# Performance work log

Hardware: AMD Instinct MI355X
Metric: run time of the kernel (lower is better)

The kernel has to match this reference:

```python
import jax, jax.numpy as jnp
import numpy as np

# FlowNetC correlation config: kernel_size=1, so no kernel-window averaging;
# pad_size == max_displacement -> output spatial size == input spatial size.
B, C, H, W = 8, 256, 48, 64
MAX_DISP = 20   # max_displacement
STRIDE2 = 2     # displacement stride
PAD = 20        # pad_size
GRID_RAD = MAX_DISP // STRIDE2            # 10
GRID_W = 2 * GRID_RAD + 1                 # 21 -> 441 displacement channels


def setup_inputs() -> dict:
    key = jax.random.key(0)
    k1, k2 = jax.random.split(key)
    return {
        "input1": jax.random.normal(k1, (B, C, H, W), dtype=jnp.float32),
        "input2": jax.random.normal(k2, (B, C, H, W), dtype=jnp.float32),
    }


def _correlation(input1, input2):
    b, c, h, w = input1.shape
    p2 = jnp.pad(input2, ((0, 0), (0, 0), (PAD, PAD), (PAD, PAD)))
    # Displacement start offsets into the padded map. dy-major ordering matches
    # the CUDA kernel: top_channel = dy_idx * GRID_W + dx_idx.
    d = np.arange(-GRID_RAD, GRID_RAD + 1) * STRIDE2 + PAD  # [21]
    offs = np.stack(np.meshgrid(d, d, indexing="ij"), axis=-1).reshape(-1, 2)
    offs = jnp.asarray(offs, dtype=jnp.int32)  # [441, 2] (dy, dx)
    sumelems = jnp.float32(c)  # kernel_size^2 * C with kernel_size=1

    def step(carry, o):
        shifted = jax.lax.dynamic_slice(p2, (0, 0, o[0], o[1]), (b, c, h, w))
        # mean over channels of elementwise product -> [B, H, W]
        return carry, jnp.sum(input1 * shifted, axis=1) / sumelems

    _, ys = jax.lax.scan(step, 0, offs)          # [441, B, H, W]
    return jnp.transpose(ys, (1, 0, 2, 3))       # [B, 441, H, W]


def reference(input1, input2):
    return _correlation(input1, input2)
```

## Files before the change

### kernel.cpp

```cpp
#include <hip/hip_runtime.h>

typedef __bf16 bf16x8 __attribute__((ext_vector_type(8)));
typedef float f32x4 __attribute__((ext_vector_type(4)));
typedef float f32x16 __attribute__((ext_vector_type(16)));

#define CC 256
#define HH 48
#define WW 64
#define HW (HH * WW)
#define NB 8
#define GW 21

__global__ __launch_bounds__(256) void prep_kernel(const float* __restrict__ in1,
                                                   const float* __restrict__ in2,
                                                   unsigned short* __restrict__ o1,
                                                   unsigned short* __restrict__ o2)
{
    __shared__ float lds[CC * 33];
    int blk  = blockIdx.x;
    int sel  = (blk >= 768);
    int blk2 = sel ? blk - 768 : blk;
    int b  = blk2 & 7;
    int st = blk2 >> 3;
    int s0 = st * 32;
    const float* src = sel ? in2 : in1;
    unsigned short* dst = sel ? o2 : o1;
    float scale = sel ? 1.0f : (1.0f / 256.0f);

    int t = threadIdx.x;
    int sidx  = t & 31;
    int cbase = t >> 5;
    const float* sb = src + (size_t)b * CC * HW + s0;
    #pragma unroll
    for (int p = 0; p < 32; ++p) {
        int c = cbase + p * 8;
        lds[c * 33 + sidx] = sb[(size_t)c * HW + sidx] * scale;
    }
    __syncthreads();

    int y  = s0 >> 6;
    int xb = s0 & 63;
    int s  = t & 31;
    int c8 = t >> 5;
    unsigned short* db = dst + (size_t)(b * HH + y) * 32 * 64 * 8;
    #pragma unroll
    for (int it = 0; it < 4; ++it) {
        int cblk = it * 8 + c8;
        unsigned dw[4];
        #pragma unroll
        for (int d = 0; d < 4; ++d) {
            unsigned u0 = __builtin_bit_cast(unsigned, lds[(cblk * 8 + 2 * d) * 33 + s]);
            u0 += 0x7fffu + ((u0 >> 16) & 1u);
            unsigned u1 = __builtin_bit_cast(unsigned, lds[(cblk * 8 + 2 * d + 1) * 33 + s]);
            u1 += 0x7fffu + ((u1 >> 16) & 1u);
            dw[d] = (u0 >> 16) | (u1 & 0xffff0000u);
        }
        *(uint4*)(db + ((size_t)cblk * 64 + xb + s) * 8) =
            make_uint4(dw[0], dw[1], dw[2], dw[3]);
    }
}

__global__ __launch_bounds__(256, 4) void corr_kernel(const unsigned short* __restrict__ in1F,
                                                      const unsigned short* __restrict__ in2F,
                                                      float* __restrict__ out)
{
    __shared__ float dbuf[4 * 2304];
    int blk  = blockIdx.x;
    int b    = blk & 7;
    int t2   = blk >> 3;
    int ysrc = (t2 % 88) - 20;
    int jg   = t2 / 88;
    int tid  = threadIdx.x;
    int w    = tid >> 6;
    int lane = tid & 63;

    int j = jg * 4 + w;
    if (j > 20) return;
    int yo = ysrc - 2 * (j - 10);
    if (yo < 0 || yo >= HH) return;

    float* orow = out + (((size_t)(b * 441 + j * GW)) * HH + yo) * WW;

    if (ysrc < 0 || ysrc >= HH) {
        #pragma unroll
        for (int jx = 0; jx < GW; ++jx)
            orow[(size_t)jx * HW + lane] = 0.0f;
        return;
    }

    int l31 = lane & 31;
    int q2  = lane >> 5;

    const unsigned short* arow =
        in1F + (((size_t)(b * HH + yo) * 32 + q2) * 64 + l31) * 8;
    const unsigned short* brow =
        in2F + (((size_t)(b * HH + ysrc) * 32 + q2) * 64 + l31) * 8;

    f32x16 acc[2][2];
    #pragma unroll
    for (int mt = 0; mt < 2; ++mt)
        #pragma unroll
        for (int nt = 0; nt < 2; ++nt)
            acc[mt][nt] = (f32x16)(0.0f);

    bf16x8 Af[2][2], Bf[2][2];
    #pragma unroll
    for (int mt = 0; mt < 2; ++mt)
        Af[0][mt] = *(const bf16x8*)(arow + mt * 32 * 8);
    #pragma unroll
    for (int nt = 0; nt < 2; ++nt)
        Bf[0][nt] = *(const bf16x8*)(brow + nt * 32 * 8);

    #pragma unroll
    for (int kk = 0; kk < 16; ++kk) {
        int cur = kk & 1, nxt = cur ^ 1;
        if (kk < 15) {
            #pragma unroll
            for (int mt = 0; mt < 2; ++mt)
                Af[nxt][mt] = *(const bf16x8*)(arow + (size_t)(kk + 1) * 1024 + mt * 32 * 8);
            #pragma unroll
            for (int nt = 0; nt < 2; ++nt)
                Bf[nxt][nt] = *(const bf16x8*)(brow + (size_t)(kk + 1) * 1024 + nt * 32 * 8);
        }
        #pragma unroll
        for (int mt = 0; mt < 2; ++mt)
            #pragma unroll
            for (int nt = 0; nt < 2; ++nt)
                acc[mt][nt] = __builtin_amdgcn_mfma_f32_32x32x16_bf16(
                    Af[cur][mt], Bf[cur][nt], acc[mt][nt], 0, 0, 0);
    }

    float* dtw = dbuf + w * 2304;
    #pragma unroll
    for (int h = 0; h < 2; ++h) {
        #pragma unroll
        for (int nt = 0; nt < 2; ++nt) {
            #pragma unroll
            for (int rq = 0; rq < 4; ++rq) {
                f32x4 v = { acc[h][nt][4 * rq], acc[h][nt][4 * rq + 1],
                            acc[h][nt][4 * rq + 2], acc[h][nt][4 * rq + 3] };
                *(f32x4*)(dtw + (nt * 32 + l31) * 36 + rq * 8 + q2 * 4) = v;
            }
        }
        int x = h * 32 + l31;
        #pragma unroll
        for (int jj = 0; jj < 11; ++jj) {
            int jx = 2 * jj + q2;
            if (jx >= GW) continue;
            int colx = x + 2 * (jx - 10);
            float v = (colx >= 0 && colx < WW) ? dtw[colx * 36 + l31] : 0.0f;
            orow[(size_t)jx * HW + x] = v;
        }
    }
}

extern "C" void kernel_launch(void* const* d_in, const int* in_sizes, int n_in,
                              void* d_out, int out_size, void* d_ws, size_t ws_size,
                              hipStream_t stream)
{
    (void)in_sizes; (void)n_in; (void)out_size; (void)ws_size;
    const float* in1 = (const float*)d_in[0];
    const float* in2 = (const float*)d_in[1];
    float* out = (float*)d_out;

    unsigned short* in1F = (unsigned short*)d_ws;
    unsigned short* in2F = in1F + (size_t)NB * HW * CC;

    prep_kernel<<<dim3(1536), dim3(256), 0, stream>>>(in1, in2, in1F, in2F);
    corr_kernel<<<dim3(NB * 88 * 6), dim3(256), 0, stream>>>(in1F, in2F, out);
}
```

Baseline: 118.4 us.

## Stage shared input2 row in LDS, deepen A prefetch, use nontemporal stores

All four waves in a block share the same input2 row, so that 32KB row is now loaded cooperatively into LDS once per block and the B fragments are read from LDS instead of global memory. The A operand prefetch is deepened to three buffers to hide more global latency. Output stores become nontemporal to avoid polluting the cache. The change adds two block-wide barriers, keeps invalid waves alive until those barriers, and reuses the same LDS for the transpose staging.

```diff
diff --git a/kernel.cpp b/kernel.cpp
--- a/kernel.cpp
+++ b/kernel.cpp
@@ -64,7 +64,9 @@
                                                       const unsigned short* __restrict__ in2F,
                                                       float* __restrict__ out)
 {
-    __shared__ float dbuf[4 * 2304];
+    __shared__ unsigned char smem[36864];
+    unsigned short* Bl = (unsigned short*)smem;
+
     int blk  = blockIdx.x;
     int b    = blk & 7;
     int t2   = blk >> 3;
@@ -74,63 +76,86 @@
     int w    = tid >> 6;
     int lane = tid & 63;
 
-    int j = jg * 4 + w;
-    if (j > 20) return;
+    int j  = jg * 4 + w;
     int yo = ysrc - 2 * (j - 10);
-    if (yo < 0 || yo >= HH) return;
+    bool jvalid = (j <= 20) && (yo >= 0) && (yo < HH);
 
-    float* orow = out + (((size_t)(b * 441 + j * GW)) * HH + yo) * WW;
+    float* orow = jvalid
+        ? out + (((size_t)(b * 441 + j * GW)) * HH + yo) * WW
+        : out;
 
     if (ysrc < 0 || ysrc >= HH) {
-        #pragma unroll
-        for (int jx = 0; jx < GW; ++jx)
-            orow[(size_t)jx * HW + lane] = 0.0f;
+        if (jvalid) {
+            #pragma unroll
+            for (int jx = 0; jx < GW; ++jx)
+                __builtin_nontemporal_store(0.0f, orow + (size_t)jx * HW + lane);
+        }
         return;
     }
+
+    {
+        const unsigned short* bsrc = in2F + (size_t)(b * HH + ysrc) * (32 * 64 * 8);
+        #pragma unroll
+        for (int it = 0; it < 8; ++it) {
+            size_t off = ((size_t)it * 256 + tid) * 8;
+            *(uint4*)(Bl + off) = *(const uint4*)(bsrc + off);
+        }
+    }
+    __syncthreads();
 
     int l31 = lane & 31;
     int q2  = lane >> 5;
 
-    const unsigned short* arow =
-        in1F + (((size_t)(b * HH + yo) * 32 + q2) * 64 + l31) * 8;
-    const unsigned short* brow =
-        in2F + (((size_t)(b * HH + ysrc) * 32 + q2) * 64 + l31) * 8;
+    f32x16 acc[2][2];
+    if (jvalid) {
+        const unsigned short* arow =
+            in1F + (((size_t)(b * HH + yo) * 32 + q2) * 64 + l31) * 8;
+        const unsigned short* brow = Bl + ((size_t)q2 * 64 + l31) * 8;
 
-    f32x16 acc[2][2];
-    #pragma unroll
-    for (int mt = 0; mt < 2; ++mt)
-        #pragma unroll
-        for (int nt = 0; nt < 2; ++nt)
-            acc[mt][nt] = (f32x16)(0.0f);
-
-    bf16x8 Af[2][2], Bf[2][2];
-    #pragma unroll
-    for (int mt = 0; mt < 2; ++mt)
-        Af[0][mt] = *(const bf16x8*)(arow + mt * 32 * 8);
-    #pragma unroll
-    for (int nt = 0; nt < 2; ++nt)
-        Bf[0][nt] = *(const bf16x8*)(brow + nt * 32 * 8);
-
-    #pragma unroll
-    for (int kk = 0; kk < 16; ++kk) {
-        int cur = kk & 1, nxt = cur ^ 1;
-        if (kk < 15) {
-            #pragma unroll
-            for (int mt = 0; mt < 2; ++mt)
-                Af[nxt][mt] = *(const bf16x8*)(arow + (size_t)(kk + 1) * 1024 + mt * 32 * 8);
-            #pragma unroll
-            for (int nt = 0; nt < 2; ++nt)
-                Bf[nxt][nt] = *(const bf16x8*)(brow + (size_t)(kk + 1) * 1024 + nt * 32 * 8);
-        }
         #pragma unroll
         for (int mt = 0; mt < 2; ++mt)
             #pragma unroll
             for (int nt = 0; nt < 2; ++nt)
-                acc[mt][nt] = __builtin_amdgcn_mfma_f32_32x32x16_bf16(
-                    Af[cur][mt], Bf[cur][nt], acc[mt][nt], 0, 0, 0);
+                acc[mt][nt] = (f32x16)(0.0f);
+
+        bf16x8 Ab[3][2], Bb[2][2];
+        #pragma unroll
+        for (int mt = 0; mt < 2; ++mt) {
+            Ab[0][mt] = *(const bf16x8*)(arow + mt * 256);
+            Ab[1][mt] = *(const bf16x8*)(arow + 1024 + mt * 256);
+        }
+        #pragma unroll
+        for (int nt = 0; nt < 2; ++nt)
+            Bb[0][nt] = *(const bf16x8*)(brow + nt * 256);
+
+        #pragma unroll
+        for (int kk = 0; kk < 16; ++kk) {
+            if (kk < 14) {
+                #pragma unroll
+                for (int mt = 0; mt < 2; ++mt)
+                    Ab[(kk + 2) % 3][mt] =
+                        *(const bf16x8*)(arow + (size_t)(kk + 2) * 1024 + mt * 256);
+            }
+            if (kk < 15) {
+                #pragma unroll
+                for (int nt = 0; nt < 2; ++nt)
+                    Bb[(kk + 1) & 1][nt] =
+                        *(const bf16x8*)(brow + (size_t)(kk + 1) * 1024 + nt * 256);
+            }
+            #pragma unroll
+            for (int mt = 0; mt < 2; ++mt)
+                #pragma unroll
+                for (int nt = 0; nt < 2; ++nt)
+                    acc[mt][nt] = __builtin_amdgcn_mfma_f32_32x32x16_bf16(
+                        Ab[kk % 3][mt], Bb[kk & 1][nt], acc[mt][nt], 0, 0, 0);
+        }
     }
 
-    float* dtw = dbuf + w * 2304;
+    __syncthreads();
+
+    if (!jvalid) return;
+
+    float* dtw = (float*)smem + w * 2304;
     #pragma unroll
     for (int h = 0; h < 2; ++h) {
         #pragma unroll
@@ -149,7 +174,7 @@
             if (jx >= GW) continue;
             int colx = x + 2 * (jx - 10);
             float v = (colx >= 0 && colx < WW) ? dtw[colx * 36 + l31] : 0.0f;
-            orow[(size_t)jx * HW + x] = v;
+            __builtin_nontemporal_store(v, orow + (size_t)jx * HW + x);
         }
     }
 }
```

New measurement: 118.3 us. About the same (-0.1%).
